# Optimization experiments

Hardware: AMD Instinct MI355X
Metric: run time of the kernel (lower is better)

The kernel has to match this reference:

```python
import jax, jax.numpy as jnp
import numpy as np

B, C, N, H, W = 4, 64, 32, 64, 64
S = C // 2  # shurink


def setup_inputs() -> dict:
    key = jax.random.key(0)
    ks = jax.random.split(key, 18)

    def w(k, shape):
        fan_in = shape[-1]
        return (jax.random.normal(k, shape, jnp.float32) * (2.0 / fan_in) ** 0.5).astype(jnp.float32)

    def b(k, n):
        return jax.random.normal(k, (n,), jnp.float32) * 0.01

    return {
        "x": jax.random.normal(ks[0], (B, C, N, H, W), jnp.float32),
        "light": jax.random.normal(ks[1], (B, 3, N), jnp.float32),
        # 1x1x1 Conv3d projections == channel matmuls
        "wk": w(ks[2], (S, C)), "bk": b(ks[3], S),
        "wq": w(ks[4], (S, C)), "bq": b(ks[5], S),
        "wv": w(ks[6], (S, C)), "bv": b(ks[7], S),
        "wo": w(ks[8], (C - 3, S)), "bo": b(ks[9], C - 3),
        # light_emb: three 1x1 Conv2d layers 3 -> S//4 -> S//2 -> S
        "lw1": w(ks[10], (S // 4, 3)), "lb1": b(ks[11], S // 4),
        "lw2": w(ks[12], (S // 2, S // 4)), "lb2": b(ks[13], S // 2),
        "lw3": w(ks[14], (S, S // 2)), "lb3": b(ks[15], S),
    }


def reference(x, light, wk, bk, wq, bq, wv, bv, wo, bo, lw1, lb1, lw2, lb2, lw3, lb3):
    Bv, Cv, Nv, Hv, Wv = x.shape
    Sv = wk.shape[0]
    scale = 1.0 / jnp.sqrt(jnp.asarray(Sv, x.dtype))

    # light positional embedding: pairwise light-direction differences
    lp = jnp.concatenate([light, -jnp.ones_like(light[:, :, :1])], axis=2)  # [B,3,M]
    diff = lp[:, :, :, None] - lp[:, :, None, :]                            # [B,3,M,M]
    h = jax.nn.leaky_relu(jnp.einsum('oc,bcij->boij', lw1, diff) + lb1[None, :, None, None], 0.1)
    h = jax.nn.leaky_relu(jnp.einsum('oc,bcij->boij', lw2, h) + lb2[None, :, None, None], 0.1)
    le = jnp.einsum('oc,bcij->boij', lw3, h) + lb3[None, :, None, None]     # [B,S,M,M]

    # extra token: max-pool over the observation axis, prepended
    extra = jnp.max(x, axis=2, keepdims=True)          # [B,C,1,H,W]
    x = jnp.concatenate([extra, x], axis=2)            # [B,C,M,H,W], M=N+1

    # fused 1x1x1 conv projections, laid out [B,H,W,S,M]
    kt = jnp.einsum('sc,bcmhw->bhwsm', wk, x) + bk[None, None, None, :, None]
    qt = jnp.einsum('sc,bcmhw->bhwsm', wq, x) + bq[None, None, None, :, None]
    vt = jnp.einsum('sc,bcmhw->bhwsm', wv, x) + bv[None, None, None, :, None]

    # scores[b,h,w,i,j] = sum_s k[s,i] q[s,j]; softmax over key index i (dim=1 of bmm result)
    scores = jnp.einsum('bhwsi,bhwsj->bhwij', kt, qt) * scale
    a = jax.nn.softmax(scores, axis=-2)
    # additive light bias from query x light embedding
    a = a + jnp.einsum('bhwsk,bskg->bhwkg', qt, le)
    # value aggregation
    o = jnp.einsum('bhwsm,bhwmg->bhwsg', vt, a)        # [B,H,W,S,M]
    # output 1x1x1 conv to C-3 channels
    ao = jnp.einsum('os,bhwsm->bomhw', wo, o) + bo[None, :, None, None, None]

    # residual into the last C-3 channels (atten_factor = 1)
    x = x.at[:, 3:].add(ao)
    return x[:, :, 1:]
```

## Files before the change

### kernel.cpp

```cpp
#include <hip/hip_runtime.h>
#include <stdint.h>

#define TB 512
#define SCALE 0.17677669529663687f

typedef __attribute__((ext_vector_type(8))) short short8;
typedef __attribute__((ext_vector_type(4))) float f32x4;
#define MFMA(a, b, c) __builtin_amdgcn_mfma_f32_16x16x32_bf16(a, b, c, 0, 0, 0)

__device__ __forceinline__ float bf2f(uint16_t u) {
    union { uint32_t i; float f; } v; v.i = ((uint32_t)u) << 16; return v.f;
}
__device__ __forceinline__ uint16_t f2bf(float f) {
    union { float f; uint32_t i; } v; v.f = f;
    uint32_t r = v.i + 0x7fffu + ((v.i >> 16) & 1u);
    return (uint16_t)(r >> 16);
}
__device__ __forceinline__ int swz(int n, int c)  { return (n << 6) + (c ^ ((n & 7) << 3)); }
__device__ __forceinline__ int wswz(int q, int c) { return (q << 6) + (c ^ ((q & 7) << 3)); }
__device__ __forceinline__ int oswz(int oc, int s){ return (oc << 5) + (s ^ ((oc & 3) << 3)); }

__global__ void light_emb_kernel(const float* __restrict__ light,
                                 const float* __restrict__ lw1, const float* __restrict__ lb1,
                                 const float* __restrict__ lw2, const float* __restrict__ lb2,
                                 const float* __restrict__ lw3, const float* __restrict__ lb3,
                                 uint16_t* __restrict__ le) {
    int e = blockIdx.x * 256 + threadIdx.x;
    if (e >= 4 * 33 * 33) return;
    int j = e % 33;
    int i = (e / 33) % 33;
    int b = e / (33 * 33);
    float d[3];
    #pragma unroll
    for (int c = 0; c < 3; ++c) {
        float a  = (i < 32) ? light[(b * 3 + c) * 32 + i] : -1.0f;
        float bb = (j < 32) ? light[(b * 3 + c) * 32 + j] : -1.0f;
        d[c] = a - bb;
    }
    float h1[8];
    #pragma unroll
    for (int o = 0; o < 8; ++o) {
        float s = lb1[o];
        #pragma unroll
        for (int c = 0; c < 3; ++c) s += lw1[o * 3 + c] * d[c];
        h1[o] = (s >= 0.f) ? s : 0.1f * s;
    }
    float h2[16];
    #pragma unroll
    for (int o = 0; o < 16; ++o) {
        float s = lb2[o];
        #pragma unroll
        for (int c = 0; c < 8; ++c) s += lw2[o * 8 + c] * h1[c];
        h2[o] = (s >= 0.f) ? s : 0.1f * s;
    }
    uint16_t* dst = le + (size_t)e * 32;
    #pragma unroll
    for (int o = 0; o < 32; ++o) {
        float s = lb3[o];
        #pragma unroll
        for (int c = 0; c < 16; ++c) s += lw3[o * 16 + c] * h2[c];
        dst[o] = f2bf(s);
    }
}

#define ARENA_SZ 7840
#define WBUF_OFF 62720
#define WOL_OFF  75008
#define BIAS_OFF 79104
#define BOL_OFF  79488
#define POOL_SZ  79744

__global__ void __launch_bounds__(TB, 4)
fused_attn_kernel(const float* __restrict__ x,
                  const float* __restrict__ wk, const float* __restrict__ bk,
                  const float* __restrict__ wq, const float* __restrict__ bq,
                  const float* __restrict__ wv, const float* __restrict__ bv,
                  const float* __restrict__ wo, const float* __restrict__ bo,
                  const uint16_t* __restrict__ le,
                  float* __restrict__ out) {
    __shared__ __align__(16) unsigned char pool[POOL_SZ];
    uint16_t* xs   = (uint16_t*)pool;
    uint16_t* wbuf = (uint16_t*)(pool + WBUF_OFF);
    uint16_t* wol  = (uint16_t*)(pool + WOL_OFF);
    float*    bias = (float*)(pool + BIAS_OFF);
    float*    bol  = (float*)(pool + BOL_OFF);

    const int t = threadIdx.x;
    const int i_  = blockIdx.x;
    const int w0  = ((i_ >> 3) & 7) << 3;
    const int bh  = ((i_ >> 6) << 3) | (i_ & 7);
    const int b   = bh >> 6;
    const int h   = bh & 63;

    const int lane = t & 63, px = t >> 6;
    const int lrow = lane & 15;
    const int lk   = (lane >> 4) << 3;
    const int drow = (lane >> 4) << 2;

    uint16_t* kT = (uint16_t*)(pool + px * ARENA_SZ);
    uint16_t* qT = kT + 1320;
    uint16_t* v2 = kT + 2640;
    uint16_t* ao = qT;

    for (int e = t; e < 96 * 64; e += TB) {
        int q = e >> 6, c = e & 63;
        float v = (q < 32) ? wk[e] : (q < 64) ? wq[e - 2048] : wv[e - 4096];
        wbuf[wswz(q, c)] = f2bf(v);
    }
    if (t < 96) bias[t] = (t < 32) ? bk[t] : (t < 64) ? bq[t - 32] : bv[t - 64];
    for (int e = t; e < 64 * 32; e += TB) {
        int oc = e >> 5, s = e & 31;
        wol[oswz(oc, s)] = (oc < 61) ? f2bf(wo[oc * 32 + s]) : (uint16_t)0;
    }
    if (t < 64) bol[t] = (t < 61) ? bo[t] : 0.f;
    {
        const int fh = t & 1;
        #pragma unroll
        for (int it = 0; it < 8; ++it) {
            int p = (t >> 1) + it * 256;
            int c = p >> 5, m = p & 31;
            const float4 xv = *(const float4*)&x[(((size_t)(b * 64 + c) * 32 + m) * 64 + h) * 64 + w0 + fh * 4];
            #pragma unroll
            for (int q = 0; q < 4; ++q) {
                int pxx = fh * 4 + q;
                xs[swz(pxx * 33 + m + 1, c)] = f2bf(((const float*)&xv)[q]);
            }
        }
    }
    __syncthreads();

    {
        const int c = lane;
        float mx = bf2f(xs[swz(px * 33 + 1, c)]);
        #pragma unroll
        for (int m = 2; m <= 32; ++m) mx = fmaxf(mx, bf2f(xs[swz(px * 33 + m, c)]));
        xs[swz(px * 33, c)] = f2bf(mx);
    }

    short8 af[6][2], bfr[3][2];
    #pragma unroll
    for (int mt = 0; mt < 6; ++mt) {
        af[mt][0] = *(const short8*)&wbuf[wswz(mt * 16 + lrow, lk)];
        af[mt][1] = *(const short8*)&wbuf[wswz(mt * 16 + lrow, 32 + lk)];
    }
    #pragma unroll
    for (int nt = 0; nt < 3; ++nt) {
        int n = px * 33 + nt * 16 + lrow;
        bfr[nt][0] = *(const short8*)&xs[swz(n, lk)];
        bfr[nt][1] = *(const short8*)&xs[swz(n, 32 + lk)];
    }
    __syncthreads();

    #pragma unroll
    for (int mt = 0; mt < 6; ++mt) {
        int q0 = mt * 16 + drow;
        #pragma unroll
        for (int nt = 0; nt < 3; ++nt) {
            f32x4 acc = { bias[q0], bias[q0 + 1], bias[q0 + 2], bias[q0 + 3] };
            acc = MFMA(af[mt][0], bfr[nt][0], acc);
            acc = MFMA(af[mt][1], bfr[nt][1], acc);
            int m = nt * 16 + lrow;
            if (m <= 32) {
                if (q0 < 32) {
                    *(ushort4*)&kT[m * 40 + q0] =
                        make_ushort4(f2bf(acc[0]), f2bf(acc[1]), f2bf(acc[2]), f2bf(acc[3]));
                } else if (q0 < 64) {
                    *(ushort4*)&qT[m * 40 + (q0 - 32)] =
                        make_ushort4(f2bf(acc[0]), f2bf(acc[1]), f2bf(acc[2]), f2bf(acc[3]));
                } else {
                    #pragma unroll
                    for (int r = 0; r < 4; ++r)
                        v2[(q0 - 64 + r) * 40 + m] = f2bf(acc[r]);
                }
            }
        }
    }

    {
        short8 ka[3], qb[2];
        #pragma unroll
        for (int mt = 0; mt < 3; ++mt) ka[mt] = *(const short8*)&kT[(mt * 16 + lrow) * 40 + lk];
        #pragma unroll
        for (int jh = 0; jh < 2; ++jh) qb[jh] = *(const short8*)&qT[(1 + jh * 16 + lrow) * 40 + lk];
        f32x4 sa[3][2];
        #pragma unroll
        for (int mt = 0; mt < 3; ++mt)
            #pragma unroll
            for (int jh = 0; jh < 2; ++jh) {
                f32x4 z = { 0.f, 0.f, 0.f, 0.f };
                sa[mt][jh] = MFMA(ka[mt], qb[jh], z);
            }
        uint16_t* sc = kT;
        #pragma unroll
        for (int jh = 0; jh < 2; ++jh) {
            int jp = jh * 16 + lrow;
            #pragma unroll
            for (int mt = 0; mt < 2; ++mt) {
                int i0 = mt * 16 + drow;
                *(ushort4*)&sc[jp * 40 + i0] =
                    make_ushort4(f2bf(sa[mt][jh][0]), f2bf(sa[mt][jh][1]),
                                 f2bf(sa[mt][jh][2]), f2bf(sa[mt][jh][3]));
            }
            if (drow == 0) sc[jp * 40 + 32] = f2bf(sa[2][jh][0]);
        }
    }

    {
        uint16_t* sc = kT;
        const int jp = lane & 31, hi = lane >> 5;
        const int ib = hi ? 16 : 0;
        float v[17];
        #pragma unroll
        for (int g = 0; g < 4; ++g) {
            ushort4 u = *(const ushort4*)&sc[jp * 40 + ib + g * 4];
            v[g * 4 + 0] = bf2f(u.x); v[g * 4 + 1] = bf2f(u.y);
            v[g * 4 + 2] = bf2f(u.z); v[g * 4 + 3] = bf2f(u.w);
        }
        if (hi) v[16] = bf2f(sc[jp * 40 + 32]);
        float mx = v[0];
        #pragma unroll
        for (int k = 1; k < 16; ++k) mx = fmaxf(mx, v[k]);
        if (hi) mx = fmaxf(mx, v[16]);
        mx = fmaxf(mx, __shfl_xor(mx, 32, 64));
        float sum = 0.f;
        #pragma unroll
        for (int k = 0; k < 16; ++k) { v[k] = __expf((v[k] - mx) * SCALE); sum += v[k]; }
        if (hi) { v[16] = __expf((v[16] - mx) * SCALE); sum += v[16]; }
        sum += __shfl_xor(sum, 32, 64);
        float r = 1.0f / sum;
        #pragma unroll
        for (int g = 0; g < 4; ++g) {
            *(ushort4*)&sc[jp * 40 + ib + g * 4] =
                make_ushort4(f2bf(v[g * 4 + 0] * r), f2bf(v[g * 4 + 1] * r),
                             f2bf(v[g * 4 + 2] * r), f2bf(v[g * 4 + 3] * r));
        }
        if (hi) sc[jp * 40 + 32] = f2bf(v[16] * r);
    }
    __syncthreads();

    {
        const uint16_t* leb = le + (size_t)b * (33 * 33 * 32);
        const int pxs = lrow & 7;
        const uint16_t* qsrc = (const uint16_t*)(pool + pxs * ARENA_SZ) + 1320;
        #pragma unroll
        for (int qi = 0; qi < 4; ++qi) {
            int k = px * 4 + qi;
            short8 aq = *(const short8*)&qsrc[k * 40 + lk];
            short8 b0 = *(const short8*)&leb[(k * 33 + 1 + lrow) * 32 + lk];
            short8 b1 = *(const short8*)&leb[(k * 33 + 17 + lrow) * 32 + lk];
            f32x4 z = { 0.f, 0.f, 0.f, 0.f };
            f32x4 r0 = MFMA(aq, b0, z);
            f32x4 r1 = MFMA(aq, b1, z);
            if (lane < 32) {
                #pragma unroll
                for (int r = 0; r < 4; ++r) {
                    int pxd = drow + r;
                    uint16_t* scp = (uint16_t*)(pool + pxd * ARENA_SZ);
                    int o0 = lrow * 40 + k, o1 = (16 + lrow) * 40 + k;
                    scp[o0] = f2bf(bf2f(scp[o0]) + r0[r]);
                    scp[o1] = f2bf(bf2f(scp[o1]) + r1[r]);
                }
            }
        }
        if (px == 0) {
            const int k = 32;
            short8 aq = *(const short8*)&qsrc[k * 40 + lk];
            short8 b0 = *(const short8*)&leb[(k * 33 + 1 + lrow) * 32 + lk];
            short8 b1 = *(const short8*)&leb[(k * 33 + 17 + lrow) * 32 + lk];
            f32x4 z = { 0.f, 0.f, 0.f, 0.f };
            f32x4 r0 = MFMA(aq, b0, z);
            f32x4 r1 = MFMA(aq, b1, z);
            if (lane < 32) {
                #pragma unroll
                for (int r = 0; r < 4; ++r) {
                    int pxd = drow + r;
                    uint16_t* scp = (uint16_t*)(pool + pxd * ARENA_SZ);
                    int o0 = lrow * 40 + k, o1 = (16 + lrow) * 40 + k;
                    scp[o0] = f2bf(bf2f(scp[o0]) + r0[r]);
                    scp[o1] = f2bf(bf2f(scp[o1]) + r1[r]);
                }
            }
        }
    }
    __syncthreads();

    {
        uint16_t* abf = kT;
        short8 va[2], bb[2];
        #pragma unroll
        for (int st = 0; st < 2; ++st) va[st] = *(const short8*)&v2[(st * 16 + lrow) * 40 + lk];
        #pragma unroll
        for (int jt = 0; jt < 2; ++jt) bb[jt] = *(const short8*)&abf[(jt * 16 + lrow) * 40 + lk];
        f32x4 oacc[2][2];
        #pragma unroll
        for (int st = 0; st < 2; ++st)
            #pragma unroll
            for (int jt = 0; jt < 2; ++jt) {
                f32x4 z = { 0.f, 0.f, 0.f, 0.f };
                oacc[st][jt] = MFMA(va[st], bb[jt], z);
            }
        float a32[2], vt[2][4];
        #pragma unroll
        for (int jt = 0; jt < 2; ++jt) a32[jt] = bf2f(abf[(jt * 16 + lrow) * 40 + 32]);
        #pragma unroll
        for (int st = 0; st < 2; ++st)
            #pragma unroll
            for (int r = 0; r < 4; ++r) vt[st][r] = bf2f(v2[(st * 16 + drow + r) * 40 + 32]);
        uint16_t* ob = kT;
        #pragma unroll
        for (int st = 0; st < 2; ++st)
            #pragma unroll
            for (int jt = 0; jt < 2; ++jt) {
                #pragma unroll
                for (int r = 0; r < 4; ++r) oacc[st][jt][r] += vt[st][r] * a32[jt];
                int s0 = st * 16 + drow, jp = jt * 16 + lrow;
                *(ushort4*)&ob[jp * 40 + s0] =
                    make_ushort4(f2bf(oacc[st][jt][0]), f2bf(oacc[st][jt][1]),
                                 f2bf(oacc[st][jt][2]), f2bf(oacc[st][jt][3]));
            }
    }

    {
        uint16_t* ob = kT;
        short8 wa[4], obf[2];
        #pragma unroll
        for (int ot = 0; ot < 4; ++ot) wa[ot] = *(const short8*)&wol[oswz(ot * 16 + lrow, lk)];
        #pragma unroll
        for (int jt = 0; jt < 2; ++jt) obf[jt] = *(const short8*)&ob[(jt * 16 + lrow) * 40 + lk];
        #pragma unroll
        for (int ot = 0; ot < 4; ++ot) {
            int oc0 = ot * 16 + drow;
            #pragma unroll
            for (int jt = 0; jt < 2; ++jt) {
                f32x4 acc = { bol[oc0], bol[oc0 + 1], bol[oc0 + 2], bol[oc0 + 3] };
                acc = MFMA(wa[ot], obf[jt], acc);
                int jp = jt * 16 + lrow;
                *(ushort4*)&ao[(jp << 6) + (oc0 ^ ((jp & 7) << 3))] =
                    make_ushort4(f2bf(acc[0]), f2bf(acc[1]), f2bf(acc[2]), f2bf(acc[3]));
            }
        }
    }
    __syncthreads();

    {
        const int wpx = t & 7, m = (t >> 3) & 31, cq = t >> 8;
        const uint16_t* aop = (const uint16_t*)(pool + wpx * ARENA_SZ) + 1320;
        const size_t obase = (((size_t)(b * 64 + cq * 32) * 32 + m) << 12) + (size_t)h * 64 + w0 + wpx;
        #pragma unroll
        for (int k = 0; k < 32; ++k) {
            int c = cq * 32 + k;
            float f = x[obase + (size_t)k * 131072];
            if (c >= 3) f += bf2f(aop[(m << 6) + ((c - 3) ^ ((m & 7) << 3))]);
            out[obase + (size_t)k * 131072] = f;
        }
    }
}

extern "C" void kernel_launch(void* const* d_in, const int* in_sizes, int n_in,
                              void* d_out, int out_size, void* d_ws, size_t ws_size,
                              hipStream_t stream) {
    const float* x     = (const float*)d_in[0];
    const float* light = (const float*)d_in[1];
    const float* wk  = (const float*)d_in[2];
    const float* bk  = (const float*)d_in[3];
    const float* wq  = (const float*)d_in[4];
    const float* bq  = (const float*)d_in[5];
    const float* wv  = (const float*)d_in[6];
    const float* bv  = (const float*)d_in[7];
    const float* wo  = (const float*)d_in[8];
    const float* bo  = (const float*)d_in[9];
    const float* lw1 = (const float*)d_in[10];
    const float* lb1 = (const float*)d_in[11];
    const float* lw2 = (const float*)d_in[12];
    const float* lb2 = (const float*)d_in[13];
    const float* lw3 = (const float*)d_in[14];
    const float* lb3 = (const float*)d_in[15];
    float* out   = (float*)d_out;
    uint16_t* le = (uint16_t*)d_ws;

    light_emb_kernel<<<dim3((4 * 33 * 33 + 255) / 256), dim3(256), 0, stream>>>(
        light, lw1, lb1, lw2, lb2, lw3, lb3, le);
    fused_attn_kernel<<<dim3(2048), dim3(TB), 0, stream>>>(
        x, wk, bk, wq, bq, wv, bv, wo, bo, le, out);
}
```

Baseline: 122.4 us.

## Halve pixels per block and load QKV weight fragments directly from global

Each block now handles 4 pixels with 256 threads instead of 8 pixels with 512, and the grid doubles to 4096 blocks. The QKV weight staging buffer in LDS is removed: each wave loads its MFMA A-fragments straight from global memory and converts them to bf16 in registers. The x load is restructured so each thread packs 4 channels into one ushort4 LDS write. Together these roughly halve LDS per block to allow more resident blocks, at the cost of redundant weight loads per wave and lower coalescing on the 16-byte x reads.

```diff
diff --git a/kernel.cpp b/kernel.cpp
--- a/kernel.cpp
+++ b/kernel.cpp
@@ -1,7 +1,7 @@
 #include <hip/hip_runtime.h>
 #include <stdint.h>
 
-#define TB 512
+#define TB 256
 #define SCALE 0.17677669529663687f
 
 typedef __attribute__((ext_vector_type(8))) short short8;
@@ -17,7 +17,6 @@
     return (uint16_t)(r >> 16);
 }
 __device__ __forceinline__ int swz(int n, int c)  { return (n << 6) + (c ^ ((n & 7) << 3)); }
-__device__ __forceinline__ int wswz(int q, int c) { return (q << 6) + (c ^ ((q & 7) << 3)); }
 __device__ __forceinline__ int oswz(int oc, int s){ return (oc << 5) + (s ^ ((oc & 3) << 3)); }
 
 __global__ void light_emb_kernel(const float* __restrict__ light,
@@ -64,11 +63,10 @@
 }
 
 #define ARENA_SZ 7840
-#define WBUF_OFF 62720
-#define WOL_OFF  75008
-#define BIAS_OFF 79104
-#define BOL_OFF  79488
-#define POOL_SZ  79744
+#define WOL_OFF  31360
+#define BIAS_OFF 35456
+#define BOL_OFF  35840
+#define POOL_SZ  36096
 
 __global__ void __launch_bounds__(TB, 4)
 fused_attn_kernel(const float* __restrict__ x,
@@ -80,15 +78,14 @@
                   float* __restrict__ out) {
     __shared__ __align__(16) unsigned char pool[POOL_SZ];
     uint16_t* xs   = (uint16_t*)pool;
-    uint16_t* wbuf = (uint16_t*)(pool + WBUF_OFF);
     uint16_t* wol  = (uint16_t*)(pool + WOL_OFF);
     float*    bias = (float*)(pool + BIAS_OFF);
     float*    bol  = (float*)(pool + BOL_OFF);
 
     const int t = threadIdx.x;
     const int i_  = blockIdx.x;
-    const int w0  = ((i_ >> 3) & 7) << 3;
-    const int bh  = ((i_ >> 6) << 3) | (i_ & 7);
+    const int w0  = ((i_ >> 3) & 15) << 2;
+    const int bh  = ((i_ >> 7) << 3) | (i_ & 7);
     const int b   = bh >> 6;
     const int h   = bh & 63;
 
@@ -102,29 +99,46 @@
     uint16_t* v2 = kT + 2640;
     uint16_t* ao = qT;
 
-    for (int e = t; e < 96 * 64; e += TB) {
-        int q = e >> 6, c = e & 63;
-        float v = (q < 32) ? wk[e] : (q < 64) ? wq[e - 2048] : wv[e - 4096];
-        wbuf[wswz(q, c)] = f2bf(v);
-    }
+    short8 af[6][2];
+    {
+        const float* wsel[3] = { wk, wq, wv };
+        #pragma unroll
+        for (int mt = 0; mt < 6; ++mt) {
+            const float* wp = wsel[mt >> 1] + ((mt & 1) * 16 + lrow) * 64;
+            #pragma unroll
+            for (int hf = 0; hf < 2; ++hf) {
+                float4 lo = *(const float4*)&wp[hf * 32 + lk];
+                float4 hi = *(const float4*)&wp[hf * 32 + lk + 4];
+                short8 v;
+                v[0] = f2bf(lo.x); v[1] = f2bf(lo.y); v[2] = f2bf(lo.z); v[3] = f2bf(lo.w);
+                v[4] = f2bf(hi.x); v[5] = f2bf(hi.y); v[6] = f2bf(hi.z); v[7] = f2bf(hi.w);
+                af[mt][hf] = v;
+            }
+        }
+    }
+
     if (t < 96) bias[t] = (t < 32) ? bk[t] : (t < 64) ? bq[t - 32] : bv[t - 64];
     for (int e = t; e < 64 * 32; e += TB) {
         int oc = e >> 5, s = e & 31;
         wol[oswz(oc, s)] = (oc < 61) ? f2bf(wo[oc * 32 + s]) : (uint16_t)0;
     }
     if (t < 64) bol[t] = (t < 61) ? bo[t] : 0.f;
-    {
-        const int fh = t & 1;
-        #pragma unroll
-        for (int it = 0; it < 8; ++it) {
-            int p = (t >> 1) + it * 256;
-            int c = p >> 5, m = p & 31;
-            const float4 xv = *(const float4*)&x[(((size_t)(b * 64 + c) * 32 + m) * 64 + h) * 64 + w0 + fh * 4];
-            #pragma unroll
-            for (int q = 0; q < 4; ++q) {
-                int pxx = fh * 4 + q;
-                xs[swz(pxx * 33 + m + 1, c)] = f2bf(((const float*)&xv)[q]);
-            }
+    #pragma unroll
+    for (int u = 0; u < 2; ++u) {
+        int unit = t + u * 256;
+        int cg = unit >> 5, m = unit & 31;
+        int c0 = cg * 4;
+        float4 xv[4];
+        #pragma unroll
+        for (int i = 0; i < 4; ++i)
+            xv[i] = *(const float4*)&x[(((size_t)(b * 64 + c0 + i) * 32 + m) * 64 + h) * 64 + w0];
+        #pragma unroll
+        for (int p = 0; p < 4; ++p) {
+            ushort4 pk = make_ushort4(f2bf(((const float*)&xv[0])[p]),
+                                      f2bf(((const float*)&xv[1])[p]),
+                                      f2bf(((const float*)&xv[2])[p]),
+                                      f2bf(((const float*)&xv[3])[p]));
+            *(ushort4*)&xs[swz(p * 33 + m + 1, c0)] = pk;
         }
     }
     __syncthreads();
@@ -137,12 +151,7 @@
         xs[swz(px * 33, c)] = f2bf(mx);
     }
 
-    short8 af[6][2], bfr[3][2];
-    #pragma unroll
-    for (int mt = 0; mt < 6; ++mt) {
-        af[mt][0] = *(const short8*)&wbuf[wswz(mt * 16 + lrow, lk)];
-        af[mt][1] = *(const short8*)&wbuf[wswz(mt * 16 + lrow, 32 + lk)];
-    }
+    short8 bfr[3][2];
     #pragma unroll
     for (int nt = 0; nt < 3; ++nt) {
         int n = px * 33 + nt * 16 + lrow;
@@ -240,22 +249,21 @@
 
     {
         const uint16_t* leb = le + (size_t)b * (33 * 33 * 32);
-        const int pxs = lrow & 7;
+        const int pxs = lrow & 3;
         const uint16_t* qsrc = (const uint16_t*)(pool + pxs * ARENA_SZ) + 1320;
         #pragma unroll
-        for (int qi = 0; qi < 4; ++qi) {
-            int k = px * 4 + qi;
+        for (int qi = 0; qi < 8; ++qi) {
+            int k = px * 8 + qi;
             short8 aq = *(const short8*)&qsrc[k * 40 + lk];
             short8 b0 = *(const short8*)&leb[(k * 33 + 1 + lrow) * 32 + lk];
             short8 b1 = *(const short8*)&leb[(k * 33 + 17 + lrow) * 32 + lk];
             f32x4 z = { 0.f, 0.f, 0.f, 0.f };
             f32x4 r0 = MFMA(aq, b0, z);
             f32x4 r1 = MFMA(aq, b1, z);
-            if (lane < 32) {
+            if (lane < 16) {
                 #pragma unroll
                 for (int r = 0; r < 4; ++r) {
-                    int pxd = drow + r;
-                    uint16_t* scp = (uint16_t*)(pool + pxd * ARENA_SZ);
+                    uint16_t* scp = (uint16_t*)(pool + r * ARENA_SZ);
                     int o0 = lrow * 40 + k, o1 = (16 + lrow) * 40 + k;
                     scp[o0] = f2bf(bf2f(scp[o0]) + r0[r]);
                     scp[o1] = f2bf(bf2f(scp[o1]) + r1[r]);
@@ -270,11 +278,10 @@
             f32x4 z = { 0.f, 0.f, 0.f, 0.f };
             f32x4 r0 = MFMA(aq, b0, z);
             f32x4 r1 = MFMA(aq, b1, z);
-            if (lane < 32) {
+            if (lane < 16) {
                 #pragma unroll
                 for (int r = 0; r < 4; ++r) {
-                    int pxd = drow + r;
-                    uint16_t* scp = (uint16_t*)(pool + pxd * ARENA_SZ);
+                    uint16_t* scp = (uint16_t*)(pool + r * ARENA_SZ);
                     int o0 = lrow * 40 + k, o1 = (16 + lrow) * 40 + k;
                     scp[o0] = f2bf(bf2f(scp[o0]) + r0[r]);
                     scp[o1] = f2bf(bf2f(scp[o1]) + r1[r]);
@@ -343,7 +350,7 @@
     __syncthreads();
 
     {
-        const int wpx = t & 7, m = (t >> 3) & 31, cq = t >> 8;
+        const int wpx = t & 3, m = (t >> 2) & 31, cq = t >> 7;
         const uint16_t* aop = (const uint16_t*)(pool + wpx * ARENA_SZ) + 1320;
         const size_t obase = (((size_t)(b * 64 + cq * 32) * 32 + m) << 12) + (size_t)h * 64 + w0 + wpx;
         #pragma unroll
@@ -380,6 +387,6 @@
 
     light_emb_kernel<<<dim3((4 * 33 * 33 + 255) / 256), dim3(256), 0, stream>>>(
         light, lw1, lb1, lw2, lb2, lw3, lb3, le);
-    fused_attn_kernel<<<dim3(2048), dim3(TB), 0, stream>>>(
+    fused_attn_kernel<<<dim3(4096), dim3(TB), 0, stream>>>(
         x, wk, bk, wq, bq, wv, bv, wo, bo, le, out);
 }
```

Result: slower. 239.3 us (+95.6%).
